# Kernel tuning notes

Hardware: AMD Instinct MI355X
Metric: run time of the kernel (lower is better)

Reference implementation:

```python
import jax, jax.numpy as jnp
import numpy as np


def setup_inputs() -> dict:
    key = jax.random.key(0)
    kq, kk, kv = jax.random.split(key, 3)
    B, H, S, D = 4, 16, 2048, 128
    return {
        "query": jax.random.normal(kq, (B, H, S, D), dtype=jnp.float32),
        "key": jax.random.normal(kk, (B, H, S, D), dtype=jnp.float32),
        "value": jax.random.normal(kv, (B, H, S, D), dtype=jnp.float32),
    }


def reference(query, key, value):
    # Faithful to RawSDP.forward with attn_mask=None, dropout_p=0, is_casual=False.
    head_dim = query.shape[-1]
    half_sqrt = jnp.asarray(np.sqrt(np.sqrt(head_dim)), dtype=query.dtype)
    q = query / half_sqrt
    k = key / half_sqrt
    # [B,H,Sq,Skv] attention logits (split scaling, as in original)
    attn_weight = jnp.einsum("bhqd,bhkd->bhqk", q, k)
    # softmax computed in float32, cast back to query dtype
    attn_weight = jax.nn.softmax(attn_weight.astype(jnp.float32), axis=-1).astype(query.dtype)
    return jnp.einsum("bhqk,bhkd->bhqd", attn_weight, value)
```

## Files before the change

kernel.cpp:

```cpp
#include <hip/hip_runtime.h>
#include <hip/hip_bf16.h>

typedef __attribute__((ext_vector_type(8))) short short8;
typedef __attribute__((ext_vector_type(4))) short short4_t;
typedef __attribute__((ext_vector_type(4))) float float4_t;
typedef __attribute__((ext_vector_type(16))) float float16_t;
typedef __attribute__((ext_vector_type(4))) unsigned uint4_t;
typedef __attribute__((ext_vector_type(2))) unsigned uint2_t;

#define S_LEN 2048
#define D_DIM 128
#define BQ 128
#define BK 64
#define KS_STRIDE 136
#define VT_STRIDE 72

__device__ __forceinline__ short f2bf(float f) {
    union { float f; unsigned u; } x; x.f = f;
    return (short)((x.u + 0x8000u) >> 16);
}

__device__ __forceinline__ float fast_exp2(float x) {
#if __has_builtin(__builtin_amdgcn_exp2f)
    return __builtin_amdgcn_exp2f(x);
#else
    return exp2f(x);
#endif
}

__device__ __forceinline__ unsigned cvt_pk_bf16(float lo, float hi_) {
    unsigned r;
    asm("v_cvt_pk_bf16_f32 %0, %1, %2" : "=v"(r) : "v"(lo), "v"(hi_));
    return r;
}

__device__ __forceinline__ void plswap32(unsigned a, unsigned b, unsigned &r0, unsigned &r1) {
#if __has_builtin(__builtin_amdgcn_permlane32_swap)
    uint2_t rr = __builtin_amdgcn_permlane32_swap(a, b, false, false);
    r0 = rr[0]; r1 = rr[1];
#else
    const int lo = ((threadIdx.x & 63) < 32);
    unsigned pa = (unsigned)__shfl_xor((int)a, 32);
    unsigned pb = (unsigned)__shfl_xor((int)b, 32);
    r0 = lo ? a : pb;
    r1 = lo ? pa : b;
#endif
}

__global__ void __launch_bounds__(256, 2)
attn_fwd(const float* __restrict__ Q, const float* __restrict__ K,
         const float* __restrict__ V, float* __restrict__ Out)
{
    __shared__ __align__(16) short lds_k[2][BK * KS_STRIDE];
    __shared__ __align__(16) short lds_vt[2][D_DIM * VT_STRIDE];

    const int n     = blockIdx.x;
    const int xcd   = n & 7;
    const int slot  = n >> 3;
    const int bh    = xcd + 8 * (slot >> 4);
    const int qtile = slot & 15;

    const long base = (long)bh * S_LEN * D_DIM;
    const int t    = threadIdx.x;
    const int wave = t >> 6;
    const int lane = t & 63;
    const int l31  = lane & 31;
    const int hi   = lane >> 5;

    const float qscale = 1.4426950408889634f / 11.313708498984761f;

    const int qrow0 = qtile * BQ + wave * 32;
    short8 qf[8];
#pragma unroll
    for (int d16 = 0; d16 < 8; ++d16) {
        const float* p = Q + base + (long)(qrow0 + l31) * D_DIM + 16 * d16 + 8 * hi;
        float4_t a = *(const float4_t*)p;
        float4_t b = *(const float4_t*)(p + 4);
        short8 f;
        f[0] = f2bf(a[0] * qscale); f[1] = f2bf(a[1] * qscale);
        f[2] = f2bf(a[2] * qscale); f[3] = f2bf(a[3] * qscale);
        f[4] = f2bf(b[0] * qscale); f[5] = f2bf(b[1] * qscale);
        f[6] = f2bf(b[2] * qscale); f[7] = f2bf(b[3] * qscale);
        qf[d16] = f;
    }

    float16_t o[4];
#pragma unroll
    for (int dt = 0; dt < 4; ++dt)
#pragma unroll
        for (int i = 0; i < 16; ++i) o[dt][i] = 0.f;
    float lsum = 0.f;

    const int kd0 = (t & 31) << 2;
    const int ksr = t >> 5;
    const int vs  = t & 63;
    const int vdb = (t >> 6) * 32;
    float4_t kbuf[8], vbuf[8];

#pragma unroll
    for (int r = 0; r < 8; ++r)
        kbuf[r] = *(const float4_t*)(K + base + (long)(ksr + 8 * r) * D_DIM + kd0);
#pragma unroll
    for (int r = 0; r < 8; ++r)
        vbuf[r] = *(const float4_t*)(V + base + (long)vs * D_DIM + vdb + 4 * r);
#pragma unroll
    for (int r = 0; r < 8; ++r) {
        short4_t w4;
        w4[0] = f2bf(kbuf[r][0]); w4[1] = f2bf(kbuf[r][1]);
        w4[2] = f2bf(kbuf[r][2]); w4[3] = f2bf(kbuf[r][3]);
        *(short4_t*)&lds_k[0][(ksr + 8 * r) * KS_STRIDE + kd0] = w4;
        kbuf[r] = *(const float4_t*)(K + base + (long)(BK + ksr + 8 * r) * D_DIM + kd0);
    }
#pragma unroll
    for (int r = 0; r < 8; ++r) {
        const int d0 = vdb + 4 * r;
        lds_vt[0][(d0 + 0) * VT_STRIDE + vs] = f2bf(vbuf[r][0]);
        lds_vt[0][(d0 + 1) * VT_STRIDE + vs] = f2bf(vbuf[r][1]);
        lds_vt[0][(d0 + 2) * VT_STRIDE + vs] = f2bf(vbuf[r][2]);
        lds_vt[0][(d0 + 3) * VT_STRIDE + vs] = f2bf(vbuf[r][3]);
        vbuf[r] = *(const float4_t*)(V + base + (long)(BK + vs) * D_DIM + vdb + 4 * r);
    }
    __syncthreads();

    for (int kv0 = 0; kv0 < S_LEN; kv0 += BK) {
        const int cur = (kv0 >> 6) & 1;
        const int nxt = cur ^ 1;
        const int nk2 = (kv0 + 2 * BK) & (S_LEN - 1);

#pragma unroll
        for (int r = 0; r < 8; ++r) {
            short4_t w4;
            w4[0] = f2bf(kbuf[r][0]); w4[1] = f2bf(kbuf[r][1]);
            w4[2] = f2bf(kbuf[r][2]); w4[3] = f2bf(kbuf[r][3]);
            *(short4_t*)&lds_k[nxt][(ksr + 8 * r) * KS_STRIDE + kd0] = w4;
            kbuf[r] = *(const float4_t*)(K + base + (long)(nk2 + ksr + 8 * r) * D_DIM + kd0);
        }
#pragma unroll
        for (int r = 0; r < 8; ++r) {
            const int d0 = vdb + 4 * r;
            lds_vt[nxt][(d0 + 0) * VT_STRIDE + vs] = f2bf(vbuf[r][0]);
            lds_vt[nxt][(d0 + 1) * VT_STRIDE + vs] = f2bf(vbuf[r][1]);
            lds_vt[nxt][(d0 + 2) * VT_STRIDE + vs] = f2bf(vbuf[r][2]);
            lds_vt[nxt][(d0 + 3) * VT_STRIDE + vs] = f2bf(vbuf[r][3]);
            vbuf[r] = *(const float4_t*)(V + base + (long)(nk2 + vs) * D_DIM + vdb + 4 * r);
        }

        float16_t sacc[2];
#pragma unroll
        for (int kt = 0; kt < 2; ++kt)
#pragma unroll
            for (int i = 0; i < 16; ++i) sacc[kt][i] = 0.f;
        __builtin_amdgcn_s_setprio(1);
#pragma unroll
        for (int kt = 0; kt < 2; ++kt)
#pragma unroll
            for (int d16 = 0; d16 < 8; ++d16) {
                short8 kf = *(const short8*)&lds_k[cur][(32 * kt + l31) * KS_STRIDE + 16 * d16 + 8 * hi];
                sacc[kt] = __builtin_amdgcn_mfma_f32_32x32x16_bf16(kf, qf[d16], sacc[kt], 0, 0, 0);
            }
        __builtin_amdgcn_s_setprio(0);

        unsigned pkw[2][8];
#pragma unroll
        for (int kt = 0; kt < 2; ++kt)
#pragma unroll
            for (int m = 0; m < 8; ++m) {
                float p0 = fast_exp2(sacc[kt][2 * m]);
                float p1 = fast_exp2(sacc[kt][2 * m + 1]);
                lsum += p0 + p1;
                pkw[kt][m] = cvt_pk_bf16(p0, p1);
            }
        short8 ap[4];
#pragma unroll
        for (int kt = 0; kt < 2; ++kt)
#pragma unroll
            for (int s = 0; s < 2; ++s) {
                unsigned w0, w1, w2, w3;
                plswap32(pkw[kt][4 * s + 0], pkw[kt][4 * s + 2], w0, w2);
                plswap32(pkw[kt][4 * s + 1], pkw[kt][4 * s + 3], w1, w3);
                union { uint4_t u; short8 s8; } cv;
                cv.u[0] = w0; cv.u[1] = w1; cv.u[2] = w2; cv.u[3] = w3;
                ap[2 * kt + s] = cv.s8;
            }

        __builtin_amdgcn_s_setprio(1);
#pragma unroll
        for (int ks = 0; ks < 4; ++ks)
#pragma unroll
            for (int dt = 0; dt < 4; ++dt) {
                short8 bv = *(const short8*)&lds_vt[cur][(32 * dt + l31) * VT_STRIDE + 16 * ks + 8 * hi];
                o[dt] = __builtin_amdgcn_mfma_f32_32x32x16_bf16(ap[ks], bv, o[dt], 0, 0, 0);
            }
        __builtin_amdgcn_s_setprio(0);

        __syncthreads();
    }

    float stot = lsum + __shfl_xor(lsum, 32);
    float invl = 1.0f / stot;
#pragma unroll
    for (int r = 0; r < 16; ++r) {
        const int crow = (r & 3) + 8 * (r >> 2) + 4 * hi;
        const float iv = __shfl(invl, crow);
        const int row = qrow0 + crow;
        float* po = Out + base + (long)row * D_DIM + l31;
        po[0]  = o[0][r] * iv;
        po[32] = o[1][r] * iv;
        po[64] = o[2][r] * iv;
        po[96] = o[3][r] * iv;
    }
}

extern "C" void kernel_launch(void* const* d_in, const int* in_sizes, int n_in,
                              void* d_out, int out_size, void* d_ws, size_t ws_size,
                              hipStream_t stream) {
    (void)in_sizes; (void)n_in; (void)d_ws; (void)ws_size; (void)out_size;
    const float* Q = (const float*)d_in[0];
    const float* K = (const float*)d_in[1];
    const float* V = (const float*)d_in[2];
    float* Out = (float*)d_out;
    dim3 grid(1024, 1, 1);
    dim3 block(256, 1, 1);
    attn_fwd<<<grid, block, 0, stream>>>(Q, K, V, Out);
}
```

Before: 365.4 us.

## Software-pipeline QK^T MFMA one tile ahead and skip redundant last-iteration prefetch

Moves the S=QK^T MFMA for the next KV tile to right after the barrier at the end of each iteration, so the exp/softmax VALU work of one tile can overlap with matrix work of the next. The last iteration now skips staging and loading a wrap-around tile. __syncthreads is replaced by an LDS-only waitcnt plus s_barrier, which avoids waiting on outstanding global prefetch loads. K conversion now uses packed v_cvt_pk_bf16, which rounds to nearest-even rather than the prior round-half-up trick. Costs more live registers (sacc kept across the loop boundary) under launch_bounds(256,2).

```diff
diff --git a/kernel.cpp b/kernel.cpp
--- a/kernel.cpp
+++ b/kernel.cpp
@@ -105,10 +105,10 @@
         vbuf[r] = *(const float4_t*)(V + base + (long)vs * D_DIM + vdb + 4 * r);
 #pragma unroll
     for (int r = 0; r < 8; ++r) {
-        short4_t w4;
-        w4[0] = f2bf(kbuf[r][0]); w4[1] = f2bf(kbuf[r][1]);
-        w4[2] = f2bf(kbuf[r][2]); w4[3] = f2bf(kbuf[r][3]);
-        *(short4_t*)&lds_k[0][(ksr + 8 * r) * KS_STRIDE + kd0] = w4;
+        uint2_t w;
+        w[0] = cvt_pk_bf16(kbuf[r][0], kbuf[r][1]);
+        w[1] = cvt_pk_bf16(kbuf[r][2], kbuf[r][3]);
+        *(uint2_t*)&lds_k[0][(ksr + 8 * r) * KS_STRIDE + kd0] = w;
         kbuf[r] = *(const float4_t*)(K + base + (long)(BK + ksr + 8 * r) * D_DIM + kd0);
     }
 #pragma unroll
@@ -120,45 +120,49 @@
         lds_vt[0][(d0 + 3) * VT_STRIDE + vs] = f2bf(vbuf[r][3]);
         vbuf[r] = *(const float4_t*)(V + base + (long)(BK + vs) * D_DIM + vdb + 4 * r);
     }
-    __syncthreads();
+    __asm__ volatile("s_waitcnt lgkmcnt(0)" ::: "memory");
+    __builtin_amdgcn_s_barrier();
+
+    float16_t sacc[2];
+#pragma unroll
+    for (int kt = 0; kt < 2; ++kt)
+#pragma unroll
+        for (int i = 0; i < 16; ++i) sacc[kt][i] = 0.f;
+    __builtin_amdgcn_s_setprio(1);
+#pragma unroll
+    for (int kt = 0; kt < 2; ++kt)
+#pragma unroll
+        for (int d16 = 0; d16 < 8; ++d16) {
+            short8 kf = *(const short8*)&lds_k[0][(32 * kt + l31) * KS_STRIDE + 16 * d16 + 8 * hi];
+            sacc[kt] = __builtin_amdgcn_mfma_f32_32x32x16_bf16(kf, qf[d16], sacc[kt], 0, 0, 0);
+        }
+    __builtin_amdgcn_s_setprio(0);
 
     for (int kv0 = 0; kv0 < S_LEN; kv0 += BK) {
-        const int cur = (kv0 >> 6) & 1;
-        const int nxt = cur ^ 1;
-        const int nk2 = (kv0 + 2 * BK) & (S_LEN - 1);
-
-#pragma unroll
-        for (int r = 0; r < 8; ++r) {
-            short4_t w4;
-            w4[0] = f2bf(kbuf[r][0]); w4[1] = f2bf(kbuf[r][1]);
-            w4[2] = f2bf(kbuf[r][2]); w4[3] = f2bf(kbuf[r][3]);
-            *(short4_t*)&lds_k[nxt][(ksr + 8 * r) * KS_STRIDE + kd0] = w4;
-            kbuf[r] = *(const float4_t*)(K + base + (long)(nk2 + ksr + 8 * r) * D_DIM + kd0);
+        const int cur  = (kv0 >> 6) & 1;
+        const int nxt  = cur ^ 1;
+        const bool notlast = (kv0 + BK) < S_LEN;
+
+        if (notlast) {
+            const int nk2 = (kv0 + 2 * BK) & (S_LEN - 1);
+#pragma unroll
+            for (int r = 0; r < 8; ++r) {
+                uint2_t w;
+                w[0] = cvt_pk_bf16(kbuf[r][0], kbuf[r][1]);
+                w[1] = cvt_pk_bf16(kbuf[r][2], kbuf[r][3]);
+                *(uint2_t*)&lds_k[nxt][(ksr + 8 * r) * KS_STRIDE + kd0] = w;
+                kbuf[r] = *(const float4_t*)(K + base + (long)(nk2 + ksr + 8 * r) * D_DIM + kd0);
+            }
+#pragma unroll
+            for (int r = 0; r < 8; ++r) {
+                const int d0 = vdb + 4 * r;
+                lds_vt[nxt][(d0 + 0) * VT_STRIDE + vs] = f2bf(vbuf[r][0]);
+                lds_vt[nxt][(d0 + 1) * VT_STRIDE + vs] = f2bf(vbuf[r][1]);
+                lds_vt[nxt][(d0 + 2) * VT_STRIDE + vs] = f2bf(vbuf[r][2]);
+                lds_vt[nxt][(d0 + 3) * VT_STRIDE + vs] = f2bf(vbuf[r][3]);
+                vbuf[r] = *(const float4_t*)(V + base + (long)(nk2 + vs) * D_DIM + vdb + 4 * r);
+            }
         }
-#pragma unroll
-        for (int r = 0; r < 8; ++r) {
-            const int d0 = vdb + 4 * r;
-            lds_vt[nxt][(d0 + 0) * VT_STRIDE + vs] = f2bf(vbuf[r][0]);
-            lds_vt[nxt][(d0 + 1) * VT_STRIDE + vs] = f2bf(vbuf[r][1]);
-            lds_vt[nxt][(d0 + 2) * VT_STRIDE + vs] = f2bf(vbuf[r][2]);
-            lds_vt[nxt][(d0 + 3) * VT_STRIDE + vs] = f2bf(vbuf[r][3]);
-            vbuf[r] = *(const float4_t*)(V + base + (long)(nk2 + vs) * D_DIM + vdb + 4 * r);
-        }
-
-        float16_t sacc[2];
-#pragma unroll
-        for (int kt = 0; kt < 2; ++kt)
-#pragma unroll
-            for (int i = 0; i < 16; ++i) sacc[kt][i] = 0.f;
-        __builtin_amdgcn_s_setprio(1);
-#pragma unroll
-        for (int kt = 0; kt < 2; ++kt)
-#pragma unroll
-            for (int d16 = 0; d16 < 8; ++d16) {
-                short8 kf = *(const short8*)&lds_k[cur][(32 * kt + l31) * KS_STRIDE + 16 * d16 + 8 * hi];
-                sacc[kt] = __builtin_amdgcn_mfma_f32_32x32x16_bf16(kf, qf[d16], sacc[kt], 0, 0, 0);
-            }
-        __builtin_amdgcn_s_setprio(0);
 
         unsigned pkw[2][8];
 #pragma unroll
@@ -193,7 +197,24 @@
             }
         __builtin_amdgcn_s_setprio(0);
 
-        __syncthreads();
+        if (notlast) {
+            __asm__ volatile("s_waitcnt lgkmcnt(0)" ::: "memory");
+            __builtin_amdgcn_s_barrier();
+
+#pragma unroll
+            for (int kt = 0; kt < 2; ++kt)
+#pragma unroll
+                for (int i = 0; i < 16; ++i) sacc[kt][i] = 0.f;
+            __builtin_amdgcn_s_setprio(1);
+#pragma unroll
+            for (int kt = 0; kt < 2; ++kt)
+#pragma unroll
+                for (int d16 = 0; d16 < 8; ++d16) {
+                    short8 kf = *(const short8*)&lds_k[nxt][(32 * kt + l31) * KS_STRIDE + 16 * d16 + 8 * hi];
+                    sacc[kt] = __builtin_amdgcn_mfma_f32_32x32x16_bf16(kf, qf[d16], sacc[kt], 0, 0, 0);
+                }
+            __builtin_amdgcn_s_setprio(0);
+        }
     }
 
     float stot = lsum + __shfl_xor(lsum, 32);
```

Result: slower. 422.7 us (+15.7%).
